# Kernel optimization log

Measured on AMD Instinct MI355X. Metric: run time of the kernel, lower is better.

The kernel has to match this reference:

```python
import jax, jax.numpy as jnp
import numpy as np

B, N, DIM, HID = 128, 4096, 16, 128

def _linear_init(key, fan_in, fan_out):
    # torch nn.Linear default: U(-1/sqrt(fan_in), 1/sqrt(fan_in))
    kw, kb = jax.random.split(key)
    bound = 1.0 / np.sqrt(fan_in)
    W = jax.random.uniform(kw, (fan_in, fan_out), minval=-bound, maxval=bound, dtype=jnp.float32)
    b = jax.random.uniform(kb, (fan_out,), minval=-bound, maxval=bound, dtype=jnp.float32)
    return W, b

def setup_inputs() -> dict:
    key = jax.random.key(0)
    ks = jax.random.split(key, 8)
    x = jax.random.normal(ks[0], (B, N, DIM), dtype=jnp.float32)
    adj_col = (jax.random.uniform(ks[1], (N,), dtype=jnp.float32) > 0.5).astype(jnp.float32)
    W_n2e, b_n2e = _linear_init(ks[2], 2 * DIM, HID)
    W_e2e, b_e2e = _linear_init(ks[3], HID, HID)
    W_e2n, b_e2n = _linear_init(ks[4], HID, HID)
    W_n2n, b_n2n = _linear_init(ks[5], HID, HID)
    W_out, b_out = _linear_init(ks[6], DIM + HID, DIM)
    return {"x": x, "adj_col": adj_col,
            "W_n2e": W_n2e, "b_n2e": b_n2e,
            "W_e2e": W_e2e, "b_e2e": b_e2e,
            "W_e2n": W_e2n, "b_e2n": b_e2n,
            "W_n2n": W_n2n, "b_n2n": b_n2n,
            "W_out": W_out, "b_out": b_out,
            "i": 0}

def reference(x, adj_col, W_n2e, b_n2e, W_e2e, b_e2e, W_e2n, b_e2n, W_n2n, b_n2n, W_out, b_out, i):
    starter = x                                        # [B, N, dim]
    ender = x[:, i, :][:, None, :]                     # [B, 1, dim]
    ender = jnp.broadcast_to(ender, starter.shape)     # [B, N, dim]
    h = jnp.concatenate([starter, ender], axis=2)      # [B, N, 2*dim]
    h = jax.nn.relu(h @ W_n2e + b_n2e)                 # [B, N, hid]
    h = jax.nn.relu(h @ W_e2e + b_e2e)                 # [B, N, hid]
    h = h * adj_col[None, :, None]                     # adjacency mask
    h = jnp.sum(h, axis=1)                             # [B, hid]
    h = jax.nn.relu(h @ W_e2n + b_e2n)
    h = jax.nn.relu(h @ W_n2n + b_n2n)
    h = jnp.concatenate([starter[:, i, :], h], axis=-1)  # [B, dim+hid]
    return h @ W_out + b_out                           # [B, dim]
```

## Files before the change

kernel.cpp:

```cpp
#include <hip/hip_runtime.h>
#include <hip/hip_bf16.h>

#define B_    128
#define N_    4096
#define DIM_  16
#define HID_  128
#define NT_   4
#define ROWS_ (N_ / NT_)

typedef __bf16 bf16x2 __attribute__((ext_vector_type(2)));
typedef __bf16 bf16x8 __attribute__((ext_vector_type(8)));
typedef float floatx16 __attribute__((ext_vector_type(16)));
typedef unsigned int u32;
typedef unsigned int u32x4 __attribute__((ext_vector_type(4)));

__device__ inline bf16x8 load_cvt8(const float* __restrict__ p) {
  const float4 u = *(const float4*)p;
  const float4 v = *(const float4*)(p + 4);
  bf16x8 r;
  r[0] = (__bf16)u.x; r[1] = (__bf16)u.y; r[2] = (__bf16)u.z; r[3] = (__bf16)u.w;
  r[4] = (__bf16)v.x; r[5] = (__bf16)v.y; r[6] = (__bf16)v.z; r[7] = (__bf16)v.w;
  return r;
}

__device__ inline u32 pk2(float a, float b) {
  bf16x2 p; p[0] = (__bf16)a; p[1] = (__bf16)b;
  return __builtin_bit_cast(u32, p);
}

__global__ __launch_bounds__(256, 2) void edge_kernel(
    const float* __restrict__ x, const float* __restrict__ adj,
    const float* __restrict__ W1, const float* __restrict__ b1,
    const float* __restrict__ W2, const float* __restrict__ b2,
    const int* __restrict__ ip, float* __restrict__ part)
{
  __shared__ __align__(16) __bf16 sW2[HID_ * HID_];
  __shared__ int   sIdx[ROWS_ + 192];
  __shared__ float sAcc[HID_];
  __shared__ float sB1[HID_];
  __shared__ float sEnder[DIM_];
  __shared__ int   sCnt;

  const int t  = threadIdx.x;
  const int b  = blockIdx.y;
  const int n0 = blockIdx.x * ROWS_;
  const int ii = __ldg(ip);

  const int wave = t >> 6, lane = t & 63;
  const int half = lane >> 5, l31 = lane & 31;

  if (t == 0) sCnt = 0;
  if (t < HID_) sAcc[t] = 0.f;
  if (t < DIM_) sEnder[t] = x[((size_t)b * N_ + ii) * DIM_ + t];
  __syncthreads();

  #pragma unroll
  for (int r = t; r < ROWS_; r += 256) {
    const bool act = adj[n0 + r] != 0.f;
    const unsigned long long m = __ballot(act);
    int base = 0;
    if (lane == 0) base = atomicAdd(&sCnt, __popcll(m));
    base = __shfl(base, 0);
    if (act) {
      const int pre = __builtin_amdgcn_mbcnt_hi((u32)(m >> 32),
                      __builtin_amdgcn_mbcnt_lo((u32)m, 0));
      sIdx[base + pre] = n0 + r;
    }
  }

  #pragma unroll
  for (int e = 0; e < 8; ++e) {
    const int G = t * 8 + e;
    const int c = G >> 4, gg = G & 15;
    bf16x8 v;
    #pragma unroll
    for (int j = 0; j < 8; ++j) v[j] = (__bf16)W2[((gg << 3) + j) * HID_ + c];
    *(bf16x8*)&sW2[(c << 7) + ((gg ^ (c & 15)) << 3)] = v;
  }

  bf16x8 w1f[4];
  #pragma unroll
  for (int ft = 0; ft < 4; ++ft) {
    bf16x8 v;
    #pragma unroll
    for (int j = 0; j < 8; ++j)
      v[j] = (__bf16)W1[(half * 8 + j) * HID_ + (ft * 32 + l31)];
    w1f[ft] = v;
  }

  if (t < HID_) {
    float s = b1[t];
    #pragma unroll
    for (int k = 0; k < DIM_; ++k) s += sEnder[k] * W1[(DIM_ + k) * HID_ + t];
    sB1[t] = s;
  }

  const float bv0 = b2[l31], bv1 = b2[32 + l31], bv2 = b2[64 + l31], bv3 = b2[96 + l31];

  __syncthreads();
  const int cnt = sCnt;
  const int nch = (cnt + 31) >> 5;
  const int end = nch * 32;
  for (int p = cnt + t; p < end + 160; p += 256) sIdx[p] = n0;

  bf16x8 a2f[4], onef;
  #pragma unroll
  for (int j = 0; j < 8; ++j) onef[j] = (__bf16)0.f;
  if (half == 0) { onef[0] = (__bf16)1.f; onef[1] = (__bf16)1.f; }
  #pragma unroll
  for (int ft = 0; ft < 4; ++ft) {
    bf16x8 v;
    #pragma unroll
    for (int j = 0; j < 8; ++j) v[j] = (__bf16)0.f;
    if (half == 0) {
      const float s = sB1[ft * 32 + l31];
      const __bf16 hi = (__bf16)s;
      v[0] = hi;
      v[1] = (__bf16)(s - (float)hi);
    }
    a2f[ft] = v;
  }
  __syncthreads();

  float sum0 = 0.f, sum1 = 0.f, sum2 = 0.f, sum3 = 0.f;
  floatx16 zf;
  #pragma unroll
  for (int r = 0; r < 16; ++r) zf[r] = 0.f;

  int cb = wave * 32;
  bf16x8 xf;
  {
    const int row = sIdx[cb + l31];
    xf = load_cvt8(&x[((size_t)b * N_ + row) * DIM_ + half * 8]);
  }

  for (; cb < end; cb += 128) {
    const int nrow = sIdx[cb + 128 + l31];

    bf16x8 af[8];
    #pragma unroll
    for (int ft = 0; ft < 4; ++ft) {
      floatx16 hc = __builtin_amdgcn_mfma_f32_32x32x16_bf16(w1f[ft], xf, zf, 0, 0, 0);
      hc = __builtin_amdgcn_mfma_f32_32x32x16_bf16(a2f[ft], onef, hc, 0, 0, 0);
      #pragma unroll
      for (int sg = 0; sg < 2; ++sg) {
        float e0 = fmaxf(hc[8*sg+0], 0.f), e1 = fmaxf(hc[8*sg+1], 0.f);
        float e2 = fmaxf(hc[8*sg+2], 0.f), e3 = fmaxf(hc[8*sg+3], 0.f);
        float e4 = fmaxf(hc[8*sg+4], 0.f), e5 = fmaxf(hc[8*sg+5], 0.f);
        float e6 = fmaxf(hc[8*sg+6], 0.f), e7 = fmaxf(hc[8*sg+7], 0.f);
        const u32 lo0 = pk2(e0, e1), lo1 = pk2(e2, e3);
        const u32 hi0 = pk2(e4, e5), hi1 = pk2(e6, e7);
        const u32 sA = half ? lo0 : hi0;
        const u32 sB = half ? lo1 : hi1;
        const u32 rA = (u32)__shfl_xor((int)sA, 32);
        const u32 rB = (u32)__shfl_xor((int)sB, 32);
        u32x4 d;
        d[0] = half ? rA : lo0;
        d[1] = half ? rB : lo1;
        d[2] = half ? hi0 : rA;
        d[3] = half ? hi1 : rB;
        af[ft * 2 + sg] = __builtin_bit_cast(bf16x8, d);
      }
    }

    const bf16x8 nxf = load_cvt8(&x[((size_t)b * N_ + nrow) * DIM_ + half * 8]);

    floatx16 c0 = zf, c1 = zf, c2 = zf, c3 = zf;
    #pragma unroll
    for (int s = 0; s < 8; ++s) {
      const int gp = ((s << 1) + half) ^ (l31 & 15);
      const __bf16* wp = &sW2[(l31 << 7) + (gp << 3)];
      const bf16x8 wb0 = *(const bf16x8*)(wp);
      const bf16x8 wb1 = *(const bf16x8*)(wp + (32 << 7));
      const bf16x8 wb2 = *(const bf16x8*)(wp + (64 << 7));
      const bf16x8 wb3 = *(const bf16x8*)(wp + (96 << 7));
      c0 = __builtin_amdgcn_mfma_f32_32x32x16_bf16(af[s], wb0, c0, 0, 0, 0);
      c1 = __builtin_amdgcn_mfma_f32_32x32x16_bf16(af[s], wb1, c1, 0, 0, 0);
      c2 = __builtin_amdgcn_mfma_f32_32x32x16_bf16(af[s], wb2, c2, 0, 0, 0);
      c3 = __builtin_amdgcn_mfma_f32_32x32x16_bf16(af[s], wb3, c3, 0, 0, 0);
    }

    if (cb + 32 <= cnt) {
      #pragma unroll
      for (int r = 0; r < 16; ++r) {
        sum0 += fmaxf(c0[r] + bv0, 0.f);
        sum1 += fmaxf(c1[r] + bv1, 0.f);
        sum2 += fmaxf(c2[r] + bv2, 0.f);
        sum3 += fmaxf(c3[r] + bv3, 0.f);
      }
    } else {
      #pragma unroll
      for (int r = 0; r < 16; ++r) {
        const int q = cb + (r & 3) + ((r >> 2) << 3) + (half << 2);
        if (q < cnt) {
          sum0 += fmaxf(c0[r] + bv0, 0.f);
          sum1 += fmaxf(c1[r] + bv1, 0.f);
          sum2 += fmaxf(c2[r] + bv2, 0.f);
          sum3 += fmaxf(c3[r] + bv3, 0.f);
        }
      }
    }
    xf = nxf;
  }

  sum0 += __shfl_xor(sum0, 32);
  sum1 += __shfl_xor(sum1, 32);
  sum2 += __shfl_xor(sum2, 32);
  sum3 += __shfl_xor(sum3, 32);
  if (half == 0) {
    atomicAdd(&sAcc[l31],      sum0);
    atomicAdd(&sAcc[32 + l31], sum1);
    atomicAdd(&sAcc[64 + l31], sum2);
    atomicAdd(&sAcc[96 + l31], sum3);
  }
  __syncthreads();
  if (t < HID_) part[((size_t)b * NT_ + blockIdx.x) * HID_ + t] = sAcc[t];
}

__global__ void tail_kernel(
    const float* __restrict__ x, const float* __restrict__ part,
    const float* __restrict__ W3, const float* __restrict__ b3,
    const float* __restrict__ W4, const float* __restrict__ b4,
    const float* __restrict__ W5, const float* __restrict__ b5,
    const int* __restrict__ ip, float* __restrict__ out)
{
  const int b = blockIdx.x, t = threadIdx.x;
  __shared__ float s0[HID_], s1[HID_], s2[HID_], se[DIM_];
  const int ii = __ldg(ip);
  if (t < DIM_) se[t] = x[((size_t)b * N_ + ii) * DIM_ + t];
  float a = 0.f;
  #pragma unroll
  for (int p = 0; p < NT_; ++p) a += part[((size_t)b * NT_ + p) * HID_ + t];
  s0[t] = a;
  __syncthreads();
  float v = b3[t];
  #pragma unroll 16
  for (int k = 0; k < HID_; ++k) v += s0[k] * W3[k * HID_ + t];
  s1[t] = fmaxf(v, 0.f);
  __syncthreads();
  float w = b4[t];
  #pragma unroll 16
  for (int k = 0; k < HID_; ++k) w += s1[k] * W4[k * HID_ + t];
  s2[t] = fmaxf(w, 0.f);
  __syncthreads();
  if (t < DIM_) {
    float o = b5[t];
    #pragma unroll
    for (int k = 0; k < DIM_; ++k) o += se[k] * W5[k * DIM_ + t];
    #pragma unroll 16
    for (int k = 0; k < HID_; ++k) o += s2[k] * W5[(DIM_ + k) * DIM_ + t];
    out[b * DIM_ + t] = o;
  }
}

extern "C" void kernel_launch(void* const* d_in, const int* in_sizes, int n_in,
                              void* d_out, int out_size, void* d_ws, size_t ws_size,
                              hipStream_t stream) {
  const float* x   = (const float*)d_in[0];
  const float* adj = (const float*)d_in[1];
  const float* W1  = (const float*)d_in[2];
  const float* b1  = (const float*)d_in[3];
  const float* W2  = (const float*)d_in[4];
  const float* b2  = (const float*)d_in[5];
  const float* W3  = (const float*)d_in[6];
  const float* b3  = (const float*)d_in[7];
  const float* W4  = (const float*)d_in[8];
  const float* b4  = (const float*)d_in[9];
  const float* W5  = (const float*)d_in[10];
  const float* b5  = (const float*)d_in[11];
  const int*   ip  = (const int*)d_in[12];
  float* out  = (float*)d_out;
  float* part = (float*)d_ws;

  edge_kernel<<<dim3(NT_, B_), 256, 0, stream>>>(x, adj, W1, b1, W2, b2, ip, part);
  tail_kernel<<<B_, HID_, 0, stream>>>(x, part, W3, b3, W4, b4, W5, b5, ip, out);
}
```

Measured before the change: 126.9 us.

## Software-pipeline first-layer MFMA for next chunk behind second-layer MFMAs

Restructures the edge loop so the first-layer MFMA, ReLU and bf16 repack for the next 32-row chunk run after the current chunk's second-layer MFMAs. The goal is to overlap the two dependent MFMA stages and hide the x gather latency with a prefetch distance of two chunks. The index padding grows to cover the deeper prefetch. W1 is now staged through shared memory with coalesced loads instead of strided per-lane global reads. This costs extra LDS, which may hurt the occupancy of 2 blocks per CU, and adds register pressure from holding af across iterations.

```diff
diff --git a/kernel.cpp b/kernel.cpp
--- a/kernel.cpp
+++ b/kernel.cpp
@@ -35,7 +35,8 @@
     const int* __restrict__ ip, float* __restrict__ part)
 {
   __shared__ __align__(16) __bf16 sW2[HID_ * HID_];
-  __shared__ int   sIdx[ROWS_ + 192];
+  __shared__ __align__(16) float sW1s[DIM_][HID_];
+  __shared__ int   sIdx[ROWS_ + 320];
   __shared__ float sAcc[HID_];
   __shared__ float sB1[HID_];
   __shared__ float sEnder[DIM_];
@@ -69,6 +70,9 @@
   }
 
   #pragma unroll
+  for (int e = t; e < DIM_ * HID_; e += 256) sW1s[e >> 7][e & 127] = W1[e];
+
+  #pragma unroll
   for (int e = 0; e < 8; ++e) {
     const int G = t * 8 + e;
     const int c = G >> 4, gg = G & 15;
@@ -78,16 +82,6 @@
     *(bf16x8*)&sW2[(c << 7) + ((gg ^ (c & 15)) << 3)] = v;
   }
 
-  bf16x8 w1f[4];
-  #pragma unroll
-  for (int ft = 0; ft < 4; ++ft) {
-    bf16x8 v;
-    #pragma unroll
-    for (int j = 0; j < 8; ++j)
-      v[j] = (__bf16)W1[(half * 8 + j) * HID_ + (ft * 32 + l31)];
-    w1f[ft] = v;
-  }
-
   if (t < HID_) {
     float s = b1[t];
     #pragma unroll
@@ -101,7 +95,16 @@
   const int cnt = sCnt;
   const int nch = (cnt + 31) >> 5;
   const int end = nch * 32;
-  for (int p = cnt + t; p < end + 160; p += 256) sIdx[p] = n0;
+  for (int p = cnt + t; p < end + 320; p += 256) sIdx[p] = n0;
+
+  bf16x8 w1f[4];
+  #pragma unroll
+  for (int ft = 0; ft < 4; ++ft) {
+    bf16x8 v;
+    #pragma unroll
+    for (int j = 0; j < 8; ++j) v[j] = (__bf16)sW1s[half * 8 + j][ft * 32 + l31];
+    w1f[ft] = v;
+  }
 
   bf16x8 a2f[4], onef;
   #pragma unroll
@@ -127,20 +130,18 @@
   #pragma unroll
   for (int r = 0; r < 16; ++r) zf[r] = 0.f;
 
+  bf16x8 af[8];
   int cb = wave * 32;
-  bf16x8 xf;
+
+  bf16x8 xf1;
   {
-    const int row = sIdx[cb + l31];
-    xf = load_cvt8(&x[((size_t)b * N_ + row) * DIM_ + half * 8]);
-  }
-
-  for (; cb < end; cb += 128) {
-    const int nrow = sIdx[cb + 128 + l31];
-
-    bf16x8 af[8];
+    const int row0 = sIdx[cb + l31];
+    const bf16x8 xf0 = load_cvt8(&x[((size_t)b * N_ + row0) * DIM_ + half * 8]);
+    const int row1 = sIdx[cb + 128 + l31];
+    xf1 = load_cvt8(&x[((size_t)b * N_ + row1) * DIM_ + half * 8]);
     #pragma unroll
     for (int ft = 0; ft < 4; ++ft) {
-      floatx16 hc = __builtin_amdgcn_mfma_f32_32x32x16_bf16(w1f[ft], xf, zf, 0, 0, 0);
+      floatx16 hc = __builtin_amdgcn_mfma_f32_32x32x16_bf16(w1f[ft], xf0, zf, 0, 0, 0);
       hc = __builtin_amdgcn_mfma_f32_32x32x16_bf16(a2f[ft], onef, hc, 0, 0, 0);
       #pragma unroll
       for (int sg = 0; sg < 2; ++sg) {
@@ -162,7 +163,10 @@
         af[ft * 2 + sg] = __builtin_bit_cast(bf16x8, d);
       }
     }
-
+  }
+
+  for (; cb < end; cb += 128) {
+    const int nrow = sIdx[cb + 256 + l31];
     const bf16x8 nxf = load_cvt8(&x[((size_t)b * N_ + nrow) * DIM_ + half * 8]);
 
     floatx16 c0 = zf, c1 = zf, c2 = zf, c3 = zf;
@@ -179,6 +183,32 @@
       c2 = __builtin_amdgcn_mfma_f32_32x32x16_bf16(af[s], wb2, c2, 0, 0, 0);
       c3 = __builtin_amdgcn_mfma_f32_32x32x16_bf16(af[s], wb3, c3, 0, 0, 0);
     }
+
+    #pragma unroll
+    for (int ft = 0; ft < 4; ++ft) {
+      floatx16 hc = __builtin_amdgcn_mfma_f32_32x32x16_bf16(w1f[ft], xf1, zf, 0, 0, 0);
+      hc = __builtin_amdgcn_mfma_f32_32x32x16_bf16(a2f[ft], onef, hc, 0, 0, 0);
+      #pragma unroll
+      for (int sg = 0; sg < 2; ++sg) {
+        float e0 = fmaxf(hc[8*sg+0], 0.f), e1 = fmaxf(hc[8*sg+1], 0.f);
+        float e2 = fmaxf(hc[8*sg+2], 0.f), e3 = fmaxf(hc[8*sg+3], 0.f);
+        float e4 = fmaxf(hc[8*sg+4], 0.f), e5 = fmaxf(hc[8*sg+5], 0.f);
+        float e6 = fmaxf(hc[8*sg+6], 0.f), e7 = fmaxf(hc[8*sg+7], 0.f);
+        const u32 lo0 = pk2(e0, e1), lo1 = pk2(e2, e3);
+        const u32 hi0 = pk2(e4, e5), hi1 = pk2(e6, e7);
+        const u32 sA = half ? lo0 : hi0;
+        const u32 sB = half ? lo1 : hi1;
+        const u32 rA = (u32)__shfl_xor((int)sA, 32);
+        const u32 rB = (u32)__shfl_xor((int)sB, 32);
+        u32x4 d;
+        d[0] = half ? rA : lo0;
+        d[1] = half ? rB : lo1;
+        d[2] = half ? hi0 : rA;
+        d[3] = half ? hi1 : rB;
+        af[ft * 2 + sg] = __builtin_bit_cast(bf16x8, d);
+      }
+    }
+    xf1 = nxf;
 
     if (cb + 32 <= cnt) {
       #pragma unroll
@@ -200,7 +230,6 @@
         }
       }
     }
-    xf = nxf;
   }
 
   sum0 += __shfl_xor(sum0, 32);
```

Measured after the change: 153.4 us. +20.9%, slower.
